# Performance work log

Measured on AMD Instinct MI355X. Metric: run time of the kernel, lower is better.

## Reference

```python
import jax, jax.numpy as jnp
import numpy as np

NEG_INF = -1e25


def setup_inputs() -> dict:
    key = jax.random.key(0)
    ks = jax.random.split(key, 7)
    B, L, Q, H = 4, 512, 64, 768
    bert = jax.random.normal(ks[0], (B, L, H), dtype=jnp.float32)
    query = jax.random.normal(ks[1], (B, Q, H), dtype=jnp.float32)
    mask = jax.random.randint(ks[2], (B, L), 0, 2).astype(bool)
    # nn.Linear(2H, H): weight (H, 2H), bias (H)
    W_w = jax.random.normal(ks[3], (H, 2 * H), dtype=jnp.float32) * (1.0 / np.sqrt(2 * H))
    W_b = jax.random.normal(ks[4], (H,), dtype=jnp.float32) * 0.02
    # nn.Linear(H, 1): weight (1, H), bias (1)
    v_w = jax.random.normal(ks[5], (1, H), dtype=jnp.float32) * (1.0 / np.sqrt(H))
    v_b = jax.random.normal(ks[6], (1,), dtype=jnp.float32) * 0.02
    return {"bert": bert, "query": query, "mask": mask,
            "W_w": W_w, "W_b": W_b, "v_w": v_w, "v_b": v_b}


def reference(bert, query, mask, W_w, W_b, v_w, v_b):
    H = bert.shape[-1]
    # Linear(cat([bert, query])) = bert @ Wb^T + query @ Wq^T + b  (avoids the (B,Q,L,2H) concat)
    W_bert = W_w[:, :H]    # (H, H) acts on bert part
    W_query = W_w[:, H:]   # (H, H) acts on query part
    bp = jnp.einsum('blh,kh->blk', bert, W_bert)     # (B, L, H)
    qp = jnp.einsum('bqh,kh->bqk', query, W_query)   # (B, Q, H)
    h = jnp.tanh(bp[:, None, :, :] + qp[:, :, None, :] + W_b)  # (B, Q, L, H)
    x = jnp.einsum('bqlh,h->bql', h, v_w[0]) + v_b[0]           # (B, Q, L)
    x = jnp.where(mask[:, None, :], x, NEG_INF)
    return jax.nn.softmax(x, axis=-1)
```

## Files before the change

kernel.cpp:

```cpp
#include <hip/hip_runtime.h>
#include <hip/hip_bf16.h>

#define LOG2E    1.4426950408889634f
#define TWOLOG2E 2.8853900817779268f

typedef short bf16x8 __attribute__((ext_vector_type(8)));
typedef float f32x4  __attribute__((ext_vector_type(4)));
typedef unsigned short u16x8 __attribute__((ext_vector_type(8)));

static __device__ __forceinline__ float bf16_to_f(unsigned short u) {
    union { unsigned int i; float f; } v; v.i = ((unsigned int)u) << 16; return v.f;
}
static __device__ __forceinline__ unsigned short f_to_bf16_rne(float x) {
    union { float f; unsigned int i; } v; v.f = x;
    unsigned int lsb = (v.i >> 16) & 1u;
    v.i += 0x7fffu + lsb;
    return (unsigned short)(v.i >> 16);
}

__global__ __launch_bounds__(256) void cast_frag(
    const float* __restrict__ bert, const float* __restrict__ query,
    const float* __restrict__ Ww,
    unsigned short* __restrict__ Ahf, unsigned short* __restrict__ Alf,
    unsigned short* __restrict__ Whf, unsigned short* __restrict__ Wlf)
{
    const int i    = blockIdx.x * 256 + threadIdx.x;
    const int lane = i & 63;
    const float* src;
    float scale;
    unsigned short *dh, *dl;
    size_t di;
    if (i < 221184) {
        const int rest = i >> 6;
        const int kt = rest % 24, mt = rest / 24;
        const int m  = mt * 16 + (lane & 15);
        src = ((m < 2048) ? bert + (size_t)m * 768
                          : query + (size_t)(m - 2048) * 768)
              + kt * 32 + (lane >> 4) * 8;
        scale = 1.0f;
        dh = Ahf; dl = Alf; di = (size_t)i * 8;
    } else {
        const int j = i - 221184;
        const int rest = j >> 6;
        const int kt = rest % 24, nt2 = rest / 24;
        const int sel = (nt2 >= 48) ? 1 : 0;
        const int n   = (nt2 - sel * 48) * 16 + (lane & 15);
        src = Ww + (size_t)n * 1536 + sel * 768 + kt * 32 + (lane >> 4) * 8;
        scale = TWOLOG2E;
        dh = Whf; dl = Wlf; di = (size_t)j * 8;
    }
    float4 x0 = *(const float4*)src;
    float4 x1 = *(const float4*)(src + 4);
    float xs[8] = {x0.x * scale, x0.y * scale, x0.z * scale, x0.w * scale,
                   x1.x * scale, x1.y * scale, x1.z * scale, x1.w * scale};
    u16x8 h, l;
    #pragma unroll
    for (int e = 0; e < 8; ++e) {
        unsigned short hh = f_to_bf16_rne(xs[e]);
        h[e] = hh;
        l[e] = f_to_bf16_rne(xs[e] - bf16_to_f(hh));
    }
    *(u16x8*)(dh + di) = h;
    *(u16x8*)(dl + di) = l;
}

__global__ __launch_bounds__(256) void gemm_lds(
    const unsigned short* __restrict__ Ahf, const unsigned short* __restrict__ Alf,
    const unsigned short* __restrict__ Whf, const unsigned short* __restrict__ Wlf,
    const float* __restrict__ Wb, float* __restrict__ bpT, float* __restrict__ qp)
{
    __shared__ short lds[8192];

    const int t    = threadIdx.x;
    const int w    = t >> 6;
    const int lane = t & 63;
    const int wi   = w >> 1;
    const int wj   = w & 1;
    const int lr   = lane & 15;
    const int kg   = lane >> 4;

    const int blk  = blockIdx.x;
    const int mt2  = blk / 12;
    const int nt2  = blk % 12;
    const bool isq = (mt2 >= 32);
    const int fmtA = mt2 * 4;
    const int fntB = (isq ? 48 : 0) + nt2 * 4;

    const unsigned short* gsrc[4];
    #pragma unroll
    for (int c = 0; c < 4; ++c) {
        const int r = w * 4 + c;
        if (r < 8) {
            const int f = r >> 1;
            gsrc[c] = ((r & 1) ? Alf : Ahf) + (size_t)(fmtA + f) * 12288 + lane * 8;
        } else {
            const int f = (r - 8) >> 1;
            gsrc[c] = ((r & 1) ? Wlf : Whf) + (size_t)(fntB + f) * 12288 + lane * 8;
        }
    }

    f32x4 acc[2][2];
    #pragma unroll
    for (int i = 0; i < 2; ++i)
        #pragma unroll
        for (int j = 0; j < 2; ++j) acc[i][j] = (f32x4){0.f, 0.f, 0.f, 0.f};

    for (int kt = 0; kt < 24; ++kt) {
        #pragma unroll
        for (int c = 0; c < 4; ++c) {
            const int r = w * 4 + c;
            __builtin_amdgcn_global_load_lds(
                (const __attribute__((address_space(1))) unsigned int*)(gsrc[c] + kt * 512),
                (__attribute__((address_space(3))) unsigned int*)&lds[r * 512],
                16, 0, 0);
        }
        __syncthreads();

        bf16x8 ah[2], al[2], bh[2], bl[2];
        #pragma unroll
        for (int ii = 0; ii < 2; ++ii) {
            const int a = 2 * wi + ii;
            ah[ii] = *(const bf16x8*)&lds[(a * 2 + 0) * 512 + lane * 8];
            al[ii] = *(const bf16x8*)&lds[(a * 2 + 1) * 512 + lane * 8];
        }
        #pragma unroll
        for (int jj = 0; jj < 2; ++jj) {
            const int b = 2 * wj + jj;
            bh[jj] = *(const bf16x8*)&lds[4096 + (b * 2 + 0) * 512 + lane * 8];
            bl[jj] = *(const bf16x8*)&lds[4096 + (b * 2 + 1) * 512 + lane * 8];
        }

        if (!isq) {
            #pragma unroll
            for (int ii = 0; ii < 2; ++ii)
                #pragma unroll
                for (int jj = 0; jj < 2; ++jj) {
                    acc[ii][jj] = __builtin_amdgcn_mfma_f32_16x16x32_bf16(bh[jj], ah[ii], acc[ii][jj], 0, 0, 0);
                    acc[ii][jj] = __builtin_amdgcn_mfma_f32_16x16x32_bf16(bh[jj], al[ii], acc[ii][jj], 0, 0, 0);
                    acc[ii][jj] = __builtin_amdgcn_mfma_f32_16x16x32_bf16(bl[jj], ah[ii], acc[ii][jj], 0, 0, 0);
                }
        } else {
            #pragma unroll
            for (int ii = 0; ii < 2; ++ii)
                #pragma unroll
                for (int jj = 0; jj < 2; ++jj) {
                    acc[ii][jj] = __builtin_amdgcn_mfma_f32_16x16x32_bf16(ah[ii], bh[jj], acc[ii][jj], 0, 0, 0);
                    acc[ii][jj] = __builtin_amdgcn_mfma_f32_16x16x32_bf16(ah[ii], bl[jj], acc[ii][jj], 0, 0, 0);
                    acc[ii][jj] = __builtin_amdgcn_mfma_f32_16x16x32_bf16(al[ii], bh[jj], acc[ii][jj], 0, 0, 0);
                }
        }
        __syncthreads();
    }

    const int m0 = mt2 * 64 + wi * 32;
    const int n0 = nt2 * 64 + wj * 32;
    if (!isq) {
        #pragma unroll
        for (int ii = 0; ii < 2; ++ii)
            #pragma unroll
            for (int jj = 0; jj < 2; ++jj)
                #pragma unroll
                for (int r = 0; r < 4; ++r) {
                    const int nrow = n0 + jj * 16 + kg * 4 + r;
                    const int mcol = m0 + ii * 16 + lr;
                    bpT[(size_t)nrow * 2048 + mcol] = acc[ii][jj][r];
                }
    } else {
        #pragma unroll
        for (int jj = 0; jj < 2; ++jj) {
            const int col  = n0 + jj * 16 + lr;
            const float bias = Wb[col] * TWOLOG2E;
            #pragma unroll
            for (int ii = 0; ii < 2; ++ii)
                #pragma unroll
                for (int r = 0; r < 4; ++r) {
                    const int row = m0 - 2048 + ii * 16 + kg * 4 + r;
                    qp[(size_t)row * 768 + col] = acc[ii][jj][r] + bias;
                }
        }
    }
}

__global__ __launch_bounds__(128) void attn_dense4(
    const float* __restrict__ bpT, const float* __restrict__ qp,
    const float* __restrict__ v_w, float* __restrict__ Xp)
{
    const int t   = threadIdx.x;
    const int bqt = blockIdx.x;
    const int ks  = blockIdx.y;
    const int b   = bqt >> 4;
    const int q0  = (bqt & 15) * 4;
    const int k0  = ks * 48;
    const float* bT = bpT + (size_t)b * 512 + t * 4;
    const float* pq = qp + (size_t)(b * 64 + q0) * 768;
    f32x4 acc[4];
    #pragma unroll
    for (int qi = 0; qi < 4; ++qi) acc[qi] = (f32x4){0.f, 0.f, 0.f, 0.f};

    #pragma unroll 4
    for (int k = k0; k < k0 + 48; ++k) {
        float4 bv = *(const float4*)(bT + (size_t)k * 2048);
        const float vk = v_w[k];
        float qk[4] = {pq[k], pq[768 + k], pq[1536 + k], pq[2304 + k]};
        #pragma unroll
        for (int qi = 0; qi < 4; ++qi) {
            acc[qi][0] = fmaf(vk, __builtin_amdgcn_rcpf(1.0f + __builtin_amdgcn_exp2f(bv.x + qk[qi])), acc[qi][0]);
            acc[qi][1] = fmaf(vk, __builtin_amdgcn_rcpf(1.0f + __builtin_amdgcn_exp2f(bv.y + qk[qi])), acc[qi][1]);
            acc[qi][2] = fmaf(vk, __builtin_amdgcn_rcpf(1.0f + __builtin_amdgcn_exp2f(bv.z + qk[qi])), acc[qi][2]);
            acc[qi][3] = fmaf(vk, __builtin_amdgcn_rcpf(1.0f + __builtin_amdgcn_exp2f(bv.w + qk[qi])), acc[qi][3]);
        }
    }
    #pragma unroll
    for (int qi = 0; qi < 4; ++qi)
        *(f32x4*)(Xp + (size_t)ks * 131072 + (size_t)(b * 64 + q0 + qi) * 512 + t * 4) = acc[qi];
}

__global__ __launch_bounds__(512) void softmax_mask(
    const float* __restrict__ Xp, const int* __restrict__ mask,
    float* __restrict__ out)
{
    const int bq  = blockIdx.x;
    const int b   = bq >> 6;
    const int l   = threadIdx.x;
    const int wid = l >> 6;
    __shared__ float red[8];

    const size_t idx = (size_t)bq * 512 + l;
    float v = 0.f;
    #pragma unroll
    for (int p = 0; p < 16; ++p) v += Xp[idx + (size_t)p * 131072];
    v *= -2.f;
    const bool mk = (mask[b * 512 + l] != 0);
    v = mk ? v : -1e25f;

    float m = v;
    #pragma unroll
    for (int o = 32; o; o >>= 1) m = fmaxf(m, __shfl_xor(m, o));
    if ((l & 63) == 0) red[wid] = m;
    __syncthreads();
    #pragma unroll
    for (int i = 0; i < 8; ++i) m = fmaxf(m, red[i]);

    float e = __builtin_amdgcn_exp2f((v - m) * LOG2E);
    float s = e;
    #pragma unroll
    for (int o = 32; o; o >>= 1) s += __shfl_xor(s, o);
    __syncthreads();
    if ((l & 63) == 0) red[wid] = s;
    __syncthreads();
    s = 0.f;
    #pragma unroll
    for (int i = 0; i < 8; ++i) s += red[i];

    out[idx] = e / s;
}

extern "C" void kernel_launch(void* const* d_in, const int* in_sizes, int n_in,
                              void* d_out, int out_size, void* d_ws, size_t ws_size,
                              hipStream_t stream)
{
    const float* bert  = (const float*)d_in[0];
    const float* query = (const float*)d_in[1];
    const int*   mask  = (const int*)  d_in[2];
    const float* W_w   = (const float*)d_in[3];
    const float* W_b   = (const float*)d_in[4];
    const float* v_w   = (const float*)d_in[5];
    const float* v_b   = (const float*)d_in[6];
    (void)v_b;

    float* bpT = (float*)d_ws;
    float* qp  = bpT + (size_t)768 * 2048;
    float* Xp  = qp  + (size_t)256 * 768;
    unsigned short* Ahf = (unsigned short*)(Xp + (size_t)16 * 256 * 512);
    unsigned short* Alf = Ahf + (size_t)2304 * 768;
    unsigned short* Whf = Alf + (size_t)2304 * 768;
    unsigned short* Wlf = Whf + (size_t)1536 * 768;
    float* out = (float*)d_out;

    cast_frag<<<1440, 256, 0, stream>>>(bert, query, W_w, Ahf, Alf, Whf, Wlf);
    gemm_lds<<<432, 256, 0, stream>>>(Ahf, Alf, Whf, Wlf, W_b, bpT, qp);
    attn_dense4<<<dim3(64, 16), 128, 0, stream>>>(bpT, qp, v_w, Xp);
    softmax_mask<<<dim3(256), 512, 0, stream>>>(Xp, mask, out);
}
```

Baseline: 118.7 us.

## Fuse bert projection GEMM with additive attention scoring, split qp GEMM out

Splits the GEMM into a small query-projection kernel and a bert-projection kernel that keeps its accumulator tiles in registers and directly computes the tanh/sigmoid-weighted sum over its 64-wide H slice for all 64 queries. This removes the bpT round trip through global memory and the separate attention kernel. In exchange, partial sums now go to 24 planes instead of 16, which raises the softmax reduction traffic. The fused epilogue also loops serially over 64 queries per block, with shuffles and mostly idle lanes on the stores.

Result: slower. 143.4 us (+20.8%).

```diff
diff --git a/kernel.cpp b/kernel.cpp
--- a/kernel.cpp
+++ b/kernel.cpp
@@ -16,6 +16,9 @@
     unsigned int lsb = (v.i >> 16) & 1u;
     v.i += 0x7fffu + lsb;
     return (unsigned short)(v.i >> 16);
+}
+static __device__ __forceinline__ float sigma_rcp(float x) {
+    return __builtin_amdgcn_rcpf(1.0f + __builtin_amdgcn_exp2f(x));
 }
 
 __global__ __launch_bounds__(256) void cast_frag(
@@ -64,13 +67,12 @@
     *(u16x8*)(dl + di) = l;
 }
 
-__global__ __launch_bounds__(256) void gemm_lds(
+__global__ __launch_bounds__(256) void gemm_qp(
     const unsigned short* __restrict__ Ahf, const unsigned short* __restrict__ Alf,
     const unsigned short* __restrict__ Whf, const unsigned short* __restrict__ Wlf,
-    const float* __restrict__ Wb, float* __restrict__ bpT, float* __restrict__ qp)
+    const float* __restrict__ Wb, float* __restrict__ qp)
 {
     __shared__ short lds[8192];
-
     const int t    = threadIdx.x;
     const int w    = t >> 6;
     const int lane = t & 63;
@@ -79,12 +81,10 @@
     const int lr   = lane & 15;
     const int kg   = lane >> 4;
 
-    const int blk  = blockIdx.x;
-    const int mt2  = blk / 12;
-    const int nt2  = blk % 12;
-    const bool isq = (mt2 >= 32);
-    const int fmtA = mt2 * 4;
-    const int fntB = (isq ? 48 : 0) + nt2 * 4;
+    const int mt2q = blockIdx.x / 12;
+    const int nt2  = blockIdx.x % 12;
+    const int fmtA = (32 + mt2q) * 4;
+    const int fntB = 48 + nt2 * 4;
 
     const unsigned short* gsrc[4];
     #pragma unroll
@@ -115,7 +115,6 @@
                 16, 0, 0);
         }
         __syncthreads();
-
         bf16x8 ah[2], al[2], bh[2], bl[2];
         #pragma unroll
         for (int ii = 0; ii < 2; ++ii) {
@@ -125,94 +124,152 @@
         }
         #pragma unroll
         for (int jj = 0; jj < 2; ++jj) {
-            const int b = 2 * wj + jj;
-            bh[jj] = *(const bf16x8*)&lds[4096 + (b * 2 + 0) * 512 + lane * 8];
-            bl[jj] = *(const bf16x8*)&lds[4096 + (b * 2 + 1) * 512 + lane * 8];
-        }
-
-        if (!isq) {
-            #pragma unroll
-            for (int ii = 0; ii < 2; ++ii)
-                #pragma unroll
-                for (int jj = 0; jj < 2; ++jj) {
-                    acc[ii][jj] = __builtin_amdgcn_mfma_f32_16x16x32_bf16(bh[jj], ah[ii], acc[ii][jj], 0, 0, 0);
-                    acc[ii][jj] = __builtin_amdgcn_mfma_f32_16x16x32_bf16(bh[jj], al[ii], acc[ii][jj], 0, 0, 0);
-                    acc[ii][jj] = __builtin_amdgcn_mfma_f32_16x16x32_bf16(bl[jj], ah[ii], acc[ii][jj], 0, 0, 0);
-                }
-        } else {
-            #pragma unroll
-            for (int ii = 0; ii < 2; ++ii)
-                #pragma unroll
-                for (int jj = 0; jj < 2; ++jj) {
-                    acc[ii][jj] = __builtin_amdgcn_mfma_f32_16x16x32_bf16(ah[ii], bh[jj], acc[ii][jj], 0, 0, 0);
-                    acc[ii][jj] = __builtin_amdgcn_mfma_f32_16x16x32_bf16(ah[ii], bl[jj], acc[ii][jj], 0, 0, 0);
-                    acc[ii][jj] = __builtin_amdgcn_mfma_f32_16x16x32_bf16(al[ii], bh[jj], acc[ii][jj], 0, 0, 0);
-                }
-        }
-        __syncthreads();
-    }
-
-    const int m0 = mt2 * 64 + wi * 32;
-    const int n0 = nt2 * 64 + wj * 32;
-    if (!isq) {
+            const int bb = 2 * wj + jj;
+            bh[jj] = *(const bf16x8*)&lds[4096 + (bb * 2 + 0) * 512 + lane * 8];
+            bl[jj] = *(const bf16x8*)&lds[4096 + (bb * 2 + 1) * 512 + lane * 8];
+        }
         #pragma unroll
         for (int ii = 0; ii < 2; ++ii)
             #pragma unroll
-            for (int jj = 0; jj < 2; ++jj)
-                #pragma unroll
-                for (int r = 0; r < 4; ++r) {
-                    const int nrow = n0 + jj * 16 + kg * 4 + r;
-                    const int mcol = m0 + ii * 16 + lr;
-                    bpT[(size_t)nrow * 2048 + mcol] = acc[ii][jj][r];
-                }
-    } else {
+            for (int jj = 0; jj < 2; ++jj) {
+                acc[ii][jj] = __builtin_amdgcn_mfma_f32_16x16x32_bf16(ah[ii], bh[jj], acc[ii][jj], 0, 0, 0);
+                acc[ii][jj] = __builtin_amdgcn_mfma_f32_16x16x32_bf16(ah[ii], bl[jj], acc[ii][jj], 0, 0, 0);
+                acc[ii][jj] = __builtin_amdgcn_mfma_f32_16x16x32_bf16(al[ii], bh[jj], acc[ii][jj], 0, 0, 0);
+            }
+        __syncthreads();
+    }
+
+    const int n0 = nt2 * 64 + wj * 32;
+    #pragma unroll
+    for (int jj = 0; jj < 2; ++jj) {
+        const int col  = n0 + jj * 16 + lr;
+        const float bias = Wb[col] * TWOLOG2E;
+        #pragma unroll
+        for (int ii = 0; ii < 2; ++ii)
+            #pragma unroll
+            for (int r = 0; r < 4; ++r) {
+                const int row = mt2q * 64 + wi * 32 + ii * 16 + kg * 4 + r;
+                qp[(size_t)row * 768 + col] = acc[ii][jj][r] + bias;
+            }
+    }
+}
+
+__global__ __launch_bounds__(256) void gemm_bp_attn(
+    const unsigned short* __restrict__ Ahf, const unsigned short* __restrict__ Alf,
+    const unsigned short* __restrict__ Whf, const unsigned short* __restrict__ Wlf,
+    const float* __restrict__ qp, const float* __restrict__ v_w,
+    float* __restrict__ Xp)
+{
+    __shared__ short lds[8192];
+    __shared__ float vws[64];
+    const int t    = threadIdx.x;
+    const int w    = t >> 6;
+    const int lane = t & 63;
+    const int wi   = w >> 1;
+    const int wj   = w & 1;
+    const int lr   = lane & 15;
+    const int kg   = lane >> 4;
+
+    const int mt2 = blockIdx.x / 12;
+    const int kt2 = blockIdx.x % 12;
+    const int fmtA = mt2 * 4;
+    const int fntB = kt2 * 4;
+
+    const unsigned short* gsrc[4];
+    #pragma unroll
+    for (int c = 0; c < 4; ++c) {
+        const int r = w * 4 + c;
+        if (r < 8) {
+            const int f = r >> 1;
+            gsrc[c] = ((r & 1) ? Alf : Ahf) + (size_t)(fmtA + f) * 12288 + lane * 8;
+        } else {
+            const int f = (r - 8) >> 1;
+            gsrc[c] = ((r & 1) ? Wlf : Whf) + (size_t)(fntB + f) * 12288 + lane * 8;
+        }
+    }
+
+    f32x4 acc[2][2];
+    #pragma unroll
+    for (int i = 0; i < 2; ++i)
+        #pragma unroll
+        for (int j = 0; j < 2; ++j) acc[i][j] = (f32x4){0.f, 0.f, 0.f, 0.f};
+
+    for (int kt = 0; kt < 24; ++kt) {
+        #pragma unroll
+        for (int c = 0; c < 4; ++c) {
+            const int r = w * 4 + c;
+            __builtin_amdgcn_global_load_lds(
+                (const __attribute__((address_space(1))) unsigned int*)(gsrc[c] + kt * 512),
+                (__attribute__((address_space(3))) unsigned int*)&lds[r * 512],
+                16, 0, 0);
+        }
+        __syncthreads();
+        bf16x8 ah[2], al[2], bh[2], bl[2];
+        #pragma unroll
+        for (int ii = 0; ii < 2; ++ii) {
+            const int a = 2 * wi + ii;
+            ah[ii] = *(const bf16x8*)&lds[(a * 2 + 0) * 512 + lane * 8];
+            al[ii] = *(const bf16x8*)&lds[(a * 2 + 1) * 512 + lane * 8];
+        }
         #pragma unroll
         for (int jj = 0; jj < 2; ++jj) {
-            const int col  = n0 + jj * 16 + lr;
-            const float bias = Wb[col] * TWOLOG2E;
+            const int bb = 2 * wj + jj;
+            bh[jj] = *(const bf16x8*)&lds[4096 + (bb * 2 + 0) * 512 + lane * 8];
+            bl[jj] = *(const bf16x8*)&lds[4096 + (bb * 2 + 1) * 512 + lane * 8];
+        }
+        #pragma unroll
+        for (int ii = 0; ii < 2; ++ii)
             #pragma unroll
-            for (int ii = 0; ii < 2; ++ii)
-                #pragma unroll
-                for (int r = 0; r < 4; ++r) {
-                    const int row = m0 - 2048 + ii * 16 + kg * 4 + r;
-                    qp[(size_t)row * 768 + col] = acc[ii][jj][r] + bias;
-                }
-        }
-    }
-}
-
-__global__ __launch_bounds__(128) void attn_dense4(
-    const float* __restrict__ bpT, const float* __restrict__ qp,
-    const float* __restrict__ v_w, float* __restrict__ Xp)
-{
-    const int t   = threadIdx.x;
-    const int bqt = blockIdx.x;
-    const int ks  = blockIdx.y;
-    const int b   = bqt >> 4;
-    const int q0  = (bqt & 15) * 4;
-    const int k0  = ks * 48;
-    const float* bT = bpT + (size_t)b * 512 + t * 4;
-    const float* pq = qp + (size_t)(b * 64 + q0) * 768;
-    f32x4 acc[4];
-    #pragma unroll
-    for (int qi = 0; qi < 4; ++qi) acc[qi] = (f32x4){0.f, 0.f, 0.f, 0.f};
-
-    #pragma unroll 4
-    for (int k = k0; k < k0 + 48; ++k) {
-        float4 bv = *(const float4*)(bT + (size_t)k * 2048);
-        const float vk = v_w[k];
-        float qk[4] = {pq[k], pq[768 + k], pq[1536 + k], pq[2304 + k]};
-        #pragma unroll
-        for (int qi = 0; qi < 4; ++qi) {
-            acc[qi][0] = fmaf(vk, __builtin_amdgcn_rcpf(1.0f + __builtin_amdgcn_exp2f(bv.x + qk[qi])), acc[qi][0]);
-            acc[qi][1] = fmaf(vk, __builtin_amdgcn_rcpf(1.0f + __builtin_amdgcn_exp2f(bv.y + qk[qi])), acc[qi][1]);
-            acc[qi][2] = fmaf(vk, __builtin_amdgcn_rcpf(1.0f + __builtin_amdgcn_exp2f(bv.z + qk[qi])), acc[qi][2]);
-            acc[qi][3] = fmaf(vk, __builtin_amdgcn_rcpf(1.0f + __builtin_amdgcn_exp2f(bv.w + qk[qi])), acc[qi][3]);
-        }
-    }
-    #pragma unroll
-    for (int qi = 0; qi < 4; ++qi)
-        *(f32x4*)(Xp + (size_t)ks * 131072 + (size_t)(b * 64 + q0 + qi) * 512 + t * 4) = acc[qi];
+            for (int jj = 0; jj < 2; ++jj) {
+                acc[ii][jj] = __builtin_amdgcn_mfma_f32_16x16x32_bf16(bh[jj], ah[ii], acc[ii][jj], 0, 0, 0);
+                acc[ii][jj] = __builtin_amdgcn_mfma_f32_16x16x32_bf16(bh[jj], al[ii], acc[ii][jj], 0, 0, 0);
+                acc[ii][jj] = __builtin_amdgcn_mfma_f32_16x16x32_bf16(bl[jj], ah[ii], acc[ii][jj], 0, 0, 0);
+            }
+        __syncthreads();
+    }
+
+    const int b  = (mt2 * 64) >> 9;
+    const int k0 = kt2 * 64;
+    float* qps = (float*)lds;
+    #pragma unroll
+    for (int it = 0; it < 4; ++it) {
+        const int idx = it * 256 + t;
+        const int row = idx >> 4;
+        const int col = (idx & 15) * 4;
+        *(float4*)&qps[row * 64 + col] =
+            *(const float4*)(qp + (size_t)(b * 64 + row) * 768 + k0 + col);
+    }
+    if (t < 16) *(float4*)&vws[t * 4] = *(const float4*)(v_w + k0 + t * 4);
+    __syncthreads();
+
+    const int kb = wj * 32;
+    const float4 vk0 = *(const float4*)&vws[kb + kg * 4];
+    const float4 vk1 = *(const float4*)&vws[kb + 16 + kg * 4];
+    float* xplane = Xp + (size_t)(kt2 * 2 + wj) * 131072
+                  + (size_t)(b * 64) * 512 + (mt2 & 7) * 64 + wi * 32 + lr;
+
+    for (int q = 0; q < 64; ++q) {
+        const float4 qk0 = *(const float4*)&qps[q * 64 + kb + kg * 4];
+        const float4 qk1 = *(const float4*)&qps[q * 64 + kb + 16 + kg * 4];
+        float s0 = 0.f, s1 = 0.f;
+        #pragma unroll
+        for (int r = 0; r < 4; ++r) {
+            const float v0 = ((const float*)&vk0)[r];
+            const float v1 = ((const float*)&vk1)[r];
+            const float a0 = ((const float*)&qk0)[r];
+            const float a1 = ((const float*)&qk1)[r];
+            s0 = fmaf(v0, sigma_rcp(acc[0][0][r] + a0), s0);
+            s0 = fmaf(v1, sigma_rcp(acc[0][1][r] + a1), s0);
+            s1 = fmaf(v0, sigma_rcp(acc[1][0][r] + a0), s1);
+            s1 = fmaf(v1, sigma_rcp(acc[1][1][r] + a1), s1);
+        }
+        s0 += __shfl_xor(s0, 16); s0 += __shfl_xor(s0, 32);
+        s1 += __shfl_xor(s1, 16); s1 += __shfl_xor(s1, 32);
+        if (kg == (q & 3)) {
+            xplane[(size_t)q * 512 + 0]  = s0;
+            xplane[(size_t)q * 512 + 16] = s1;
+        }
+    }
 }
 
 __global__ __launch_bounds__(512) void softmax_mask(
@@ -228,7 +285,7 @@
     const size_t idx = (size_t)bq * 512 + l;
     float v = 0.f;
     #pragma unroll
-    for (int p = 0; p < 16; ++p) v += Xp[idx + (size_t)p * 131072];
+    for (int p = 0; p < 24; ++p) v += Xp[idx + (size_t)p * 131072];
     v *= -2.f;
     const bool mk = (mask[b * 512 + l] != 0);
     v = mk ? v : -1e25f;
@@ -268,17 +325,16 @@
     const float* v_b   = (const float*)d_in[6];
     (void)v_b;
 
-    float* bpT = (float*)d_ws;
-    float* qp  = bpT + (size_t)768 * 2048;
-    float* Xp  = qp  + (size_t)256 * 768;
-    unsigned short* Ahf = (unsigned short*)(Xp + (size_t)16 * 256 * 512);
+    float* qp = (float*)d_ws;
+    float* Xp = qp + (size_t)256 * 768;
+    unsigned short* Ahf = (unsigned short*)(Xp + (size_t)24 * 256 * 512);
     unsigned short* Alf = Ahf + (size_t)2304 * 768;
     unsigned short* Whf = Alf + (size_t)2304 * 768;
     unsigned short* Wlf = Whf + (size_t)1536 * 768;
     float* out = (float*)d_out;
 
     cast_frag<<<1440, 256, 0, stream>>>(bert, query, W_w, Ahf, Alf, Whf, Wlf);
-    gemm_lds<<<432, 256, 0, stream>>>(Ahf, Alf, Whf, Wlf, W_b, bpT, qp);
-    attn_dense4<<<dim3(64, 16), 128, 0, stream>>>(bpT, qp, v_w, Xp);
+    gemm_qp<<<48, 256, 0, stream>>>(Ahf, Alf, Whf, Wlf, W_b, qp);
+    gemm_bp_attn<<<384, 256, 0, stream>>>(Ahf, Alf, Whf, Wlf, qp, v_w, Xp);
     softmax_mask<<<dim3(256), 512, 0, stream>>>(Xp, mask, out);
 }
```
